# Performance work log

Hardware: AMD Instinct MI355X
Metric: run time of the kernel (lower is better)

## Reference

```python
import jax, jax.numpy as jnp
import numpy as np
from functools import partial

EPS = 1e-5
CHANS = [(3, 64), (64, 64), (64, 128), (128, 128), (128, 256), (256, 256), (256, 256), (256, 256)]

def conv3d(x, w):
    # x: [B,X,Y,Z,Cin], w: [3,3,3,Cin,Cout]; Minkowski stride-1 conv keeps coords -> SAME padding
    return jax.lax.conv_general_dilated(x, w, window_strides=(1, 1, 1), padding='SAME',
                                        dimension_numbers=('NDHWC', 'DHWIO', 'NDHWC'))

def bn(x, g, b):
    # training-mode batch norm over all voxels (MinkowskiBatchNorm forward)
    m = jnp.mean(x, axis=(0, 1, 2, 3))
    v = jnp.var(x, axis=(0, 1, 2, 3))
    return (x - m) * jax.lax.rsqrt(v + EPS) * g + b

def maxpool2(x):
    return jax.lax.reduce_window(x, -jnp.inf, jax.lax.max,
                                 (1, 2, 2, 2, 1), (1, 2, 2, 2, 1), 'VALID')

def setup_inputs() -> dict:
    key = jax.random.key(0)
    ks = jax.random.split(key, 32)
    inp = {'x': jax.random.normal(ks[0], (2, 64, 64, 64, 3), dtype=jnp.float32)}
    for i, (ci, co) in enumerate(CHANS):
        scale = (2.0 / (27 * ci)) ** 0.5  # kaiming for 3x3x3 conv
        inp[f'w{i+1}'] = jax.random.normal(ks[1 + i], (3, 3, 3, ci, co), dtype=jnp.float32) * scale
        inp[f'g{i+1}'] = jnp.ones((co,), dtype=jnp.float32)
        inp[f'b{i+1}'] = jnp.zeros((co,), dtype=jnp.float32)
    inp['wl'] = jax.random.normal(ks[20], (256, 256), dtype=jnp.float32) * (1.0 / 16.0)
    inp['bl'] = jnp.zeros((256,), dtype=jnp.float32)
    return inp

def reference(x, w1, g1, b1, w2, g2, b2, w3, g3, b3, w4, g4, b4,
              w5, g5, b5, w6, g6, b6, w7, g7, b7, w8, g8, b8, wl, bl):
    h = jax.nn.relu(bn(conv3d(x, w1), g1, b1))
    h = jax.nn.relu(bn(conv3d(h, w2), g2, b2))
    h = maxpool2(h)                                   # 64 -> 32
    h = jax.nn.relu(bn(conv3d(h, w3), g3, b3))
    h = jax.nn.relu(bn(conv3d(h, w4), g4, b4))
    h = maxpool2(h)                                   # 32 -> 16
    h = jax.nn.relu(bn(conv3d(h, w5), g5, b5))
    h = jax.nn.relu(bn(conv3d(h, w6), g6, b6))
    h = jax.nn.relu(bn(conv3d(h, w7), g7, b7))
    h = maxpool2(h)                                   # 16 -> 8
    h = bn(conv3d(h, w8), g8, b8)                     # no ReLU before global pool in source
    h = jnp.mean(h, axis=(1, 2, 3))                   # MinkowskiGlobalPooling (avg over coords)
    return h @ wl + bl                                # MinkowskiLinear(256, out_feat)
```

## Files before the change

kernel.cpp:

```cpp
#include <hip/hip_runtime.h>


typedef _Float16 f16;
typedef _Float16 f16x8 __attribute__((ext_vector_type(8)));
typedef _Float16 f16x4 __attribute__((ext_vector_type(4)));
typedef float f32x4 __attribute__((ext_vector_type(4)));

__device__ __forceinline__ int xcd_swz(int bx, int nbx) {
  const int q = nbx >> 3, r = nbx & 7;
  const int x = bx & 7, o = bx >> 3;
  return (x < r ? x * (q + 1) : r * (q + 1) + (x - r) * q) + o;
}

struct WArgs {
  const float* src[8];
  int end[8];
  int S[8], G[8], CR[8], CO[8];
};
__global__ __launch_bounds__(256) void wprep_all(WArgs a, f16* __restrict__ wf)
{
  const int e = blockIdx.x * 256 + threadIdx.x;
  int li = 0;
  while (li < 7 && e >= a.end[li]) ++li;
  if (e >= a.end[li]) return;
  const int base = li ? a.end[li - 1] : 0;
  int x = e - base;
  const int i = x & 7;
  const int l = (x >> 3) & 63;
  int r = x >> 9;
  const int g = r % a.G[li]; r /= a.G[li];
  const int s = r % a.S[li]; r /= a.S[li];
  const int t = r;
  const int k = s * 32 + ((l >> 4) << 3) + i;
  const int co = g * 16 + (l & 15);
  const float v = (k < a.CR[li]) ? a.src[li][((long)t * a.CR[li] + k) * a.CO[li] + co] : 0.f;
  wf[e] = (f16)v;
}

template<int CIN, int CINR, int Z, int WR, int WC, bool HASBN, int SS>
__global__ __launch_bounds__(WR*WC*64) void conv_mfma(
    const void* __restrict__ xin, const f16* __restrict__ wf,
    f16* __restrict__ out, int X, int Y, int Co,
    const float* __restrict__ sc, const float* __restrict__ sh,
    float* __restrict__ part, int partBase,
    float* __restrict__ pout, long outE)
{
  constexpr int NTHR = WR * WC * 64;
  constexpr int L = 64 * WR / Z;
  constexpr int RB = (CIN + 8) * 2;
  constexpr int S = CIN / 32;
  constexpr int COW = 64 * WC;
  constexpr bool SPLIT = (SS > 0);
  __shared__ __align__(16) char slab[(L + 2) * (Z + 2) * RB];
  __shared__ float sstat[WR * WC][2][64];

  const int tid = threadIdx.x;
  const int lane = tid & 63;
  const int wv = tid >> 6;
  const int wr = wv / WC, wc = wv % WC;

  const int bxs = xcd_swz(blockIdx.x, gridDim.x);
  const long vb = (long)bxs * (64 * WR);
  const int XYZ = X * Y * Z;
  const int n = (int)(vb / XYZ);
  const int rem = (int)(vb % XYZ);
  const int x0 = rem / (Y * Z);
  const int y0 = (rem % (Y * Z)) / Z;
  const int co0 = blockIdx.y * COW;
  const int Gtot = Co >> 4;
  const int g0 = (co0 >> 4) + wc * 4;

  int abase[4];
  #pragma unroll
  for (int r = 0; r < 4; ++r) {
    const int vl = wr * 64 + r * 16 + (lane & 15);
    const int ly = vl / Z, z = vl % Z;
    abase[r] = (ly * (Z + 2) + z) * RB + ((lane >> 4) << 4);
  }

  f32x4 acc[4][4];
  const f32x4 fz = {0.f, 0.f, 0.f, 0.f};
  #pragma unroll
  for (int r = 0; r < 4; ++r)
    #pragma unroll
    for (int c = 0; c < 4; ++c) acc[r][c] = fz;

  {
    const f16x8 hz = {};
    for (int e = tid * 8; e < (L + 2) * 2 * CIN; e += NTHR * 8) {
      const int pr = e / CIN, ci = e % CIN;
      const int row = (pr >> 1) * (Z + 2) + (pr & 1) * (Z + 1);
      *(f16x8*)(slab + row * RB + ci * 2) = hz;
    }
  }

  auto stage = [&](int dx) {
    const int xs = x0 + dx - 1;
    const bool xok = (xs >= 0) && (xs < X);
    const long gv0 = ((long)(n * X + xs) * Y + (y0 - 1)) * Z;
    if constexpr (CINR == CIN) {
      const f16* xf = (const f16*)xin;
      constexpr int NE = (L + 2) * Z * CIN;
      for (int e = tid * 8; e < NE; e += NTHR * 8) {
        const int rr = e / CIN, ci = e % CIN;
        const int li = rr / Z, z = rr % Z;
        const int ys = y0 - 1 + li;
        f16x8 h = {};
        if (xok && ys >= 0 && ys < Y) {
          const f16x8 hv = *(const f16x8*)(xf + (gv0 + rr) * CIN + ci);
          if constexpr (HASBN) {
            const float4 s0 = *(const float4*)(sc + ci);
            const float4 s1 = *(const float4*)(sc + ci + 4);
            const float4 h0 = *(const float4*)(sh + ci);
            const float4 h1 = *(const float4*)(sh + ci + 4);
            h[0] = (f16)fmaxf(fmaf((float)hv[0], s0.x, h0.x), 0.f);
            h[1] = (f16)fmaxf(fmaf((float)hv[1], s0.y, h0.y), 0.f);
            h[2] = (f16)fmaxf(fmaf((float)hv[2], s0.z, h0.z), 0.f);
            h[3] = (f16)fmaxf(fmaf((float)hv[3], s0.w, h0.w), 0.f);
            h[4] = (f16)fmaxf(fmaf((float)hv[4], s1.x, h1.x), 0.f);
            h[5] = (f16)fmaxf(fmaf((float)hv[5], s1.y, h1.y), 0.f);
            h[6] = (f16)fmaxf(fmaf((float)hv[6], s1.z, h1.z), 0.f);
            h[7] = (f16)fmaxf(fmaf((float)hv[7], s1.w, h1.w), 0.f);
          } else {
            h = hv;
          }
        }
        *(f16x8*)(slab + (li * (Z + 2) + 1 + z) * RB + ci * 2) = h;
      }
    } else {
      const float* xf = (const float*)xin;
      for (int rr = tid; rr < (L + 2) * Z; rr += NTHR) {
        const int li = rr / Z, z = rr % Z;
        const int ys = y0 - 1 + li;
        f16x8 h = {};
        if (xok && ys >= 0 && ys < Y) {
          const float* p = xf + (gv0 + rr) * CINR;
          #pragma unroll
          for (int i = 0; i < CINR; ++i) h[i] = (f16)p[i];
        }
        char* drow = slab + (li * (Z + 2) + 1 + z) * RB;
        *(f16x8*)drow = h;
        const f16x8 hz = {};
        #pragma unroll
        for (int ch = 1; ch < CIN / 8; ++ch) *(f16x8*)(drow + ch * 16) = hz;
      }
    }
  };

  auto ktaps = [&](int dx, int s) {
    #pragma unroll
    for (int dy = 0; dy < 3; ++dy) {
      #pragma unroll
      for (int dzi = 0; dzi < 3; ++dzi) {
        f16x8 av[4];
        #pragma unroll
        for (int r = 0; r < 4; ++r)
          av[r] = *(const f16x8*)(slab + abase[r] + s * 64 + (dy * (Z + 2) + dzi) * RB);
        const int t = dx * 9 + dy * 3 + dzi;
        f16x8 bv[4];
        #pragma unroll
        for (int c = 0; c < 4; ++c)
          bv[c] = *(const f16x8*)((const char*)wf +
                    (((long)(t * S + s) * Gtot + g0 + c) << 10) + (lane << 4));
        #pragma unroll
        for (int r = 0; r < 4; ++r)
          #pragma unroll
          for (int c = 0; c < 4; ++c)
            acc[r][c] = __builtin_amdgcn_mfma_f32_16x16x32_f16(av[r], bv[c], acc[r][c], 0, 0, 0);
      }
    }
  };

  if constexpr (SPLIT) {
    constexpr int SCH = S / SS;
    const int zb = blockIdx.z;
    const int dx = zb / SS;
    const int s0 = (zb % SS) * SCH;
    stage(dx);
    __syncthreads();
    #pragma unroll
    for (int si = 0; si < SCH; ++si) ktaps(dx, s0 + si);
  } else {
    for (int dx = 0; dx < 3; ++dx) {
      __syncthreads();
      stage(dx);
      __syncthreads();
      for (int s = 0; s < S; ++s) ktaps(dx, s);
    }
  }

  const long vgbase = vb + wr * 64;
  const int cobase = co0 + wc * 64;
  if constexpr (SPLIT) {
    float* pb = pout + (long)blockIdx.z * outE;
    #pragma unroll
    for (int r = 0; r < 4; ++r)
      #pragma unroll
      for (int c = 0; c < 4; ++c)
        #pragma unroll
        for (int q = 0; q < 4; ++q) {
          const long vox = vgbase + r * 16 + ((lane >> 4) << 2) + q;
          const int co = cobase + c * 16 + (lane & 15);
          pb[vox * Co + co] = acc[r][c][q];
        }
    return;
  }

  #pragma unroll
  for (int r = 0; r < 4; ++r)
    #pragma unroll
    for (int c = 0; c < 4; ++c)
      #pragma unroll
      for (int q = 0; q < 4; ++q) {
        const long vox = vgbase + r * 16 + ((lane >> 4) << 2) + q;
        const int co = cobase + c * 16 + (lane & 15);
        out[vox * Co + co] = (f16)acc[r][c][q];
      }

  float s4[4], q4[4];
  #pragma unroll
  for (int c = 0; c < 4; ++c) {
    float s = 0.f, q = 0.f;
    #pragma unroll
    for (int r = 0; r < 4; ++r)
      #pragma unroll
      for (int qd = 0; qd < 4; ++qd) {
        const float v = acc[r][c][qd];
        s += v;
        q = fmaf(v, v, q);
      }
    s4[c] = s; q4[c] = q;
  }
  #pragma unroll
  for (int c = 0; c < 4; ++c) {
    s4[c] += __shfl_xor(s4[c], 16);
    s4[c] += __shfl_xor(s4[c], 32);
    q4[c] += __shfl_xor(q4[c], 16);
    q4[c] += __shfl_xor(q4[c], 32);
  }
  if (lane < 16) {
    #pragma unroll
    for (int c = 0; c < 4; ++c) {
      sstat[wv][0][c * 16 + lane] = s4[c];
      sstat[wv][1][c * 16 + lane] = q4[c];
    }
  }
  __syncthreads();
  const long entry = (long)blockIdx.y * gridDim.x + bxs + partBase;
  for (int t = tid; t < WC * 128; t += NTHR) {
    const int wcc = t >> 7, k = (t >> 6) & 1, ch = t & 63;
    float v = 0.f;
    #pragma unroll
    for (int wr2 = 0; wr2 < WR; ++wr2) v += sstat[wr2 * WC + wcc][k][ch];
    part[entry * (2 * COW) + k * COW + wcc * 64 + ch] = v;
  }
}

__global__ __launch_bounds__(256) void reduce_stats(
    const float* __restrict__ pout, f16* __restrict__ out,
    long outE, int KS, int vpb, float* __restrict__ part)
{
  const int tid = threadIdx.x;
  const int wv = tid >> 6, lane = tid & 63;
  const int vbase = blockIdx.x * vpb;
  float4 s = {0.f, 0.f, 0.f, 0.f}, q = {0.f, 0.f, 0.f, 0.f};
  for (int v = vbase + wv; v < vbase + vpb; v += 4) {
    const long e = (long)v * 256 + lane * 4;
    float4 o = *(const float4*)(pout + e);
    for (int z = 1; z < KS; ++z) {
      const float4 p = *(const float4*)(pout + (long)z * outE + e);
      o.x += p.x; o.y += p.y; o.z += p.z; o.w += p.w;
    }
    f16x4 ov = {(f16)o.x, (f16)o.y, (f16)o.z, (f16)o.w};
    *(f16x4*)(out + e) = ov;
    s.x += o.x; s.y += o.y; s.z += o.z; s.w += o.w;
    q.x = fmaf(o.x, o.x, q.x); q.y = fmaf(o.y, o.y, q.y);
    q.z = fmaf(o.z, o.z, q.z); q.w = fmaf(o.w, o.w, q.w);
  }
  __shared__ float st[4][2][256];
  *(float4*)&st[wv][0][lane * 4] = s;
  *(float4*)&st[wv][1][lane * 4] = q;
  __syncthreads();
  for (int t = tid; t < 512; t += 256) {
    const int k = t >> 8, ch = t & 255;
    part[(long)blockIdx.x * 512 + k * 256 + ch] =
        st[0][k][ch] + st[1][k][ch] + st[2][k][ch] + st[3][k][ch];
  }
}

__global__ __launch_bounds__(256) void stats_final(
    const float* __restrict__ part, int nbx, int CoWin, long nvox,
    const float* __restrict__ g, const float* __restrict__ b,
    float* __restrict__ sc, float* __restrict__ sh)
{
  const int c = blockIdx.x;
  const int by = c / CoWin;
  const int cw = c % CoWin;
  const int tid = threadIdx.x;
  float s = 0.f, ss = 0.f;
  for (int i = tid; i < nbx; i += 256) {
    const long base = ((long)by * nbx + i) * 2 * CoWin;
    s += part[base + cw];
    ss += part[base + CoWin + cw];
  }
  __shared__ float r0[256];
  __shared__ float r1[256];
  r0[tid] = s; r1[tid] = ss;
  __syncthreads();
  #pragma unroll
  for (int o = 128; o > 0; o >>= 1) {
    if (tid < o) { r0[tid] += r0[tid + o]; r1[tid] += r1[tid + o]; }
    __syncthreads();
  }
  if (tid == 0) {
    const float inv = 1.f / (float)nvox;
    const float m = r0[0] * inv;
    const float var = r1[0] * inv - m * m;
    const float scale = rsqrtf(var + 1e-5f) * g[c];
    sc[c] = scale;
    sh[c] = b[c] - m * scale;
  }
}

__global__ __launch_bounds__(256) void maxpool2_aff(
    const f16* __restrict__ in, f16* __restrict__ out,
    int N, int X, int Y, int Z, int C,
    const float* __restrict__ sc, const float* __restrict__ sh)
{
  const int OX = X >> 1, OY = Y >> 1, OZ = Z >> 1;
  const int c4n = C >> 2;
  const long nout = (long)N * OX * OY * OZ * c4n;
  long idx = (long)blockIdx.x * 256 + threadIdx.x;
  if (idx >= nout) return;
  const int c4 = (int)(idx % c4n);
  long v = idx / c4n;
  const int oz = (int)(v % OZ); v /= OZ;
  const int oy = (int)(v % OY); v /= OY;
  const int ox = (int)(v % OX);
  const int n = (int)(v / OX);
  const long sx = (long)Y * Z * C, sy = (long)Z * C, sz = C;
  const long base = ((((long)n * X + 2 * ox) * Y + 2 * oy) * Z + 2 * oz) * (long)C + 4L * c4;
  f16x4 m = *(const f16x4*)(in + base);
  #pragma unroll
  for (int dd = 1; dd < 8; ++dd) {
    const int dxp = dd >> 2, dyp = (dd >> 1) & 1, dzp = dd & 1;
    const f16x4 t = *(const f16x4*)(in + base + dxp * sx + dyp * sy + dzp * sz);
    #pragma unroll
    for (int i = 0; i < 4; ++i) m[i] = (t[i] > m[i]) ? t[i] : m[i];
  }
  const int c = 4 * c4;
  const float4 s4 = *(const float4*)(sc + c);
  const float4 h4 = *(const float4*)(sh + c);
  f16x4 r;
  r[0] = (f16)fmaxf(fmaf((float)m[0], s4.x, h4.x), 0.f);
  r[1] = (f16)fmaxf(fmaf((float)m[1], s4.y, h4.y), 0.f);
  r[2] = (f16)fmaxf(fmaf((float)m[2], s4.z, h4.z), 0.f);
  r[3] = (f16)fmaxf(fmaf((float)m[3], s4.w, h4.w), 0.f);
  *(f16x4*)(out + idx * 4) = r;
}

__global__ __launch_bounds__(256) void head_mean(
    const f16* __restrict__ x8, const float* __restrict__ sc, const float* __restrict__ sh,
    float* __restrict__ hbuf)
{
  const int n = blockIdx.x, cg = blockIdx.y;
  const int tx = threadIdx.x & 63, ty = threadIdx.x >> 6;
  const int c = cg * 64 + tx;
  float s = 0.f;
  for (int v = ty; v < 512; v += 4) s += (float)x8[((long)n * 512 + v) * 256 + c];
  __shared__ float red[4][64];
  red[ty][tx] = s;
  __syncthreads();
  if (ty == 0) {
    s = red[0][tx] + red[1][tx] + red[2][tx] + red[3][tx];
    hbuf[n * 256 + c] = fmaf(s * (1.f / 512.f), sc[c], sh[c]);
  }
}

__global__ __launch_bounds__(256) void head_mv(
    const float* __restrict__ hbuf, const float* __restrict__ wl,
    const float* __restrict__ bl, float* __restrict__ out)
{
  const int n = blockIdx.x, og = blockIdx.y;
  const int tx = threadIdx.x & 63, ty = threadIdx.x >> 6;
  const int oc = og * 64 + tx;
  float a = 0.f;
  const int k0 = ty * 64;
  for (int k = k0; k < k0 + 64; ++k)
    a = fmaf(hbuf[n * 256 + k], wl[(long)k * 256 + oc], a);
  __shared__ float red[4][64];
  red[ty][tx] = a;
  __syncthreads();
  if (ty == 0)
    out[n * 256 + oc] = red[0][tx] + red[1][tx] + red[2][tx] + red[3][tx] + bl[oc];
}

extern "C" void kernel_launch(void* const* d_in, const int* in_sizes, int n_in,
                              void* d_out, int out_size, void* d_ws, size_t ws_size,
                              hipStream_t stream)
{
  const float* x = (const float*)d_in[0];
  const float* W[8];
  const float* G[8];
  const float* B[8];
  for (int i = 0; i < 8; ++i) {
    W[i] = (const float*)d_in[1 + 3 * i];
    G[i] = (const float*)d_in[2 + 3 * i];
    B[i] = (const float*)d_in[3 + 3 * i];
  }
  const float* wl = (const float*)d_in[25];
  const float* bl = (const float*)d_in[26];

  char* ws = (char*)d_ws;
  f16*   A    = (f16*)ws;
  f16*   Bb   = (f16*)(ws + (64L << 20));
  float* pK   = (float*)(ws + (128L << 20));
  float* part = (float*)(ws + (152L << 20));
  float* scb  = part + 262144L;
  float* shb  = scb + 2048L;
  float* hbuf = shb + 2048L;
  f16*   wfb  = (f16*)(hbuf + 512L);

  const int wfS[8]  = {1, 2, 2, 4, 4, 8, 8, 8};
  const int wfG[8]  = {4, 4, 8, 8, 16, 16, 16, 16};
  const int wfCR[8] = {3, 64, 64, 128, 128, 256, 256, 256};
  const int wfCO[8] = {64, 64, 128, 128, 256, 256, 256, 256};
  long wfOff[9];
  wfOff[0] = 0;
  for (int i = 0; i < 8; ++i) wfOff[i + 1] = wfOff[i] + 27L * wfS[i] * wfG[i] * 512;
  if (ws_size < (size_t)((char*)(wfb + wfOff[8]) - ws)) return;
  auto WF = [&](int i) { return wfb + wfOff[i]; };
  auto SC = [&](int i) { return scb + i * 256; };
  auto SH = [&](int i) { return shb + i * 256; };

  {
    WArgs a;
    for (int i = 0; i < 8; ++i) {
      a.src[i] = W[i]; a.end[i] = (int)wfOff[i + 1];
      a.S[i] = wfS[i]; a.G[i] = wfG[i]; a.CR[i] = wfCR[i]; a.CO[i] = wfCO[i];
    }
    wprep_all<<<(unsigned)((wfOff[8] + 255) / 256), 256, 0, stream>>>(a, wfb);
  }

  auto fin = [&](int layer, int nbx, int CoWin, int C, long nvox) {
    stats_final<<<C, 256, 0, stream>>>(part, nbx, CoWin, nvox,
                                       G[layer], B[layer], SC(layer), SH(layer));
  };
  auto pool_aff = [&](const f16* in, f16* ob, int N, int Xd, int Yd, int Zd, int C, int layer) {
    const long nout = (long)N * (Xd / 2) * (Yd / 2) * (Zd / 2) * (C / 4);
    maxpool2_aff<<<(unsigned)((nout + 255) / 256), 256, 0, stream>>>(
        in, ob, N, Xd, Yd, Zd, C, SC(layer), SH(layer));
  };

  conv_mfma<32, 3, 64, 4, 1, false, 0><<<dim3(2048, 1), 256, 0, stream>>>(
      x, WF(0), A, 64, 64, 64, nullptr, nullptr, part, 0, nullptr, 0);
  fin(0, 2048, 64, 64, 524288);
  conv_mfma<64, 64, 64, 4, 1, true, 0><<<dim3(2048, 1), 256, 0, stream>>>(
      A, WF(1), Bb, 64, 64, 64, SC(0), SH(0), part, 0, nullptr, 0);
  fin(1, 2048, 64, 64, 524288);
  pool_aff(Bb, A, 2, 64, 64, 64, 64, 1);

  conv_mfma<64, 64, 32, 2, 2, false, 0><<<dim3(512, 1), 256, 0, stream>>>(
      A, WF(2), Bb, 32, 32, 128, nullptr, nullptr, part, 0, nullptr, 0);
  fin(2, 512, 128, 128, 65536);
  conv_mfma<128, 128, 32, 2, 2, true, 0><<<dim3(512, 1), 256, 0, stream>>>(
      Bb, WF(3), A, 32, 32, 128, SC(2), SH(2), part, 0, nullptr, 0);
  fin(3, 512, 128, 128, 65536);
  pool_aff(A, Bb, 2, 32, 32, 32, 128, 3);

  const long E16 = 2097152;
  conv_mfma<128, 128, 16, 1, 4, false, 1><<<dim3(128, 1, 3), 256, 0, stream>>>(
      Bb, WF(4), nullptr, 16, 16, 256, nullptr, nullptr, nullptr, 0, pK, E16);
  reduce_stats<<<256, 256, 0, stream>>>(pK, A, E16, 3, 32, part);
  fin(4, 256, 256, 256, 8192);
  conv_mfma<256, 256, 16, 1, 4, true, 1><<<dim3(128, 1, 3), 256, 0, stream>>>(
      A, WF(5), nullptr, 16, 16, 256, SC(4), SH(4), nullptr, 0, pK, E16);
  reduce_stats<<<256, 256, 0, stream>>>(pK, Bb, E16, 3, 32, part);
  fin(5, 256, 256, 256, 8192);
  conv_mfma<256, 256, 16, 1, 4, true, 1><<<dim3(128, 1, 3), 256, 0, stream>>>(
      Bb, WF(6), nullptr, 16, 16, 256, SC(5), SH(5), nullptr, 0, pK, E16);
  reduce_stats<<<256, 256, 0, stream>>>(pK, A, E16, 3, 32, part);
  fin(6, 256, 256, 256, 8192);
  pool_aff(A, Bb, 2, 16, 16, 16, 256, 6);

  const long E8 = 262144;
  conv_mfma<256, 256, 8, 1, 4, false, 4><<<dim3(16, 1, 12), 256, 0, stream>>>(
      Bb, WF(7), nullptr, 8, 8, 256, nullptr, nullptr, nullptr, 0, pK, E8);
  reduce_stats<<<256, 256, 0, stream>>>(pK, A, E8, 12, 4, part);
  fin(7, 256, 256, 256, 1024);

  head_mean<<<dim3(2, 4), 256, 0, stream>>>(A, SC(7), SH(7), hbuf);
  head_mv<<<dim3(2, 4), 256, 0, stream>>>(hbuf, wl, bl, (float*)d_out);
}
```

Measured before the change: 563.0 us.

## Pack first-layer conv taps into K dimension and prefetch slab staging through registers

```diff
diff --git a/kernel.cpp b/kernel.cpp
--- a/kernel.cpp
+++ b/kernel.cpp
@@ -33,13 +33,157 @@
   const int t = r;
   const int k = s * 32 + ((l >> 4) << 3) + i;
   const int co = g * 16 + (l & 15);
-  const float v = (k < a.CR[li]) ? a.src[li][((long)t * a.CR[li] + k) * a.CO[li] + co] : 0.f;
+  float v;
+  if (li == 0) {
+    const int tap = k >> 3, ci = k & 7;
+    v = (ci < 3 && tap < 27) ? a.src[0][((long)tap * 3 + ci) * 64 + co] : 0.f;
+  } else {
+    v = (k < a.CR[li]) ? a.src[li][((long)t * a.CR[li] + k) * a.CO[li] + co] : 0.f;
+  }
   wf[e] = (f16)v;
 }
 
-template<int CIN, int CINR, int Z, int WR, int WC, bool HASBN, int SS>
+__global__ __launch_bounds__(256) void conv1_mfma(
+    const float* __restrict__ xin, const f16* __restrict__ wf,
+    f16* __restrict__ out, float* __restrict__ part)
+{
+  constexpr int Z = 64, Y = 64, X = 64, L = 4;
+  constexpr int RB = 48;
+  constexpr int SLAB = (L + 2) * (Z + 2) * RB;
+  __shared__ __align__(16) char slab[3 * SLAB];
+  __shared__ float sstat[4][2][64];
+
+  const int tid = threadIdx.x;
+  const int lane = tid & 63;
+  const int wr = tid >> 6;
+
+  const int bxs = xcd_swz(blockIdx.x, gridDim.x);
+  const long vb = (long)bxs * 256;
+  const int n = (int)(vb >> 18);
+  const int rem = (int)(vb & 262143);
+  const int x0 = rem >> 12;
+  const int y0 = (rem >> 6) & 63;
+
+  if (tid < 36) {
+    const int s = tid / 12, pr = tid % 12;
+    const int row = (pr >> 1) * (Z + 2) + (pr & 1) * (Z + 1);
+    const f16x8 hz = {};
+    *(f16x8*)(slab + s * SLAB + row * RB) = hz;
+  }
+
+  for (int rr2 = tid; rr2 < 3 * (L + 2) * Z; rr2 += 256) {
+    const int s = rr2 / ((L + 2) * Z);
+    const int rr = rr2 % ((L + 2) * Z);
+    const int li = rr / Z, z = rr % Z;
+    const int xs = x0 + s - 1, ys = y0 - 1 + li;
+    f16x8 h = {};
+    if (xs >= 0 && xs < X && ys >= 0 && ys < Y) {
+      const float* p = xin + (((long)(n * X + xs) * Y + ys) * Z + z) * 3;
+      h[0] = (f16)p[0]; h[1] = (f16)p[1]; h[2] = (f16)p[2];
+    }
+    *(f16x8*)(slab + s * SLAB + (li * (Z + 2) + 1 + z) * RB) = h;
+  }
+
+  int abase[4];
+  #pragma unroll
+  for (int r = 0; r < 4; ++r) {
+    const int vl = wr * 64 + r * 16 + (lane & 15);
+    abase[r] = ((vl >> 6) * (Z + 2) + (vl & 63)) * RB;
+  }
+  const int c = lane >> 4;
+  int rofftab[7];
+  #pragma unroll
+  for (int j = 0; j < 7; ++j) {
+    const int tap = 4 * j + c;
+    if (tap < 27) {
+      const int dx = tap / 9, dy = (tap / 3) % 3, dz = tap % 3;
+      rofftab[j] = dx * SLAB + (dy * (Z + 2) + dz) * RB;
+    } else {
+      rofftab[j] = 0;
+    }
+  }
+
+  f32x4 acc[4][4];
+  const f32x4 fz = {0.f, 0.f, 0.f, 0.f};
+  #pragma unroll
+  for (int r = 0; r < 4; ++r)
+    #pragma unroll
+    for (int cc = 0; cc < 4; ++cc) acc[r][cc] = fz;
+
+  __syncthreads();
+
+  #pragma unroll
+  for (int j = 0; j < 7; ++j) {
+    f16x8 av[4];
+    #pragma unroll
+    for (int r = 0; r < 4; ++r)
+      av[r] = *(const f16x8*)(slab + abase[r] + rofftab[j]);
+    f16x8 bv[4];
+    #pragma unroll
+    for (int c2 = 0; c2 < 4; ++c2)
+      bv[c2] = *(const f16x8*)((const char*)wf + ((j * 4 + c2) << 10) + (lane << 4));
+    __builtin_amdgcn_s_setprio(1);
+    #pragma unroll
+    for (int r = 0; r < 4; ++r)
+      #pragma unroll
+      for (int c2 = 0; c2 < 4; ++c2)
+        acc[r][c2] = __builtin_amdgcn_mfma_f32_16x16x32_f16(av[r], bv[c2], acc[r][c2], 0, 0, 0);
+    __builtin_amdgcn_s_setprio(0);
+  }
+
+  const long vgbase = vb + wr * 64;
+  #pragma unroll
+  for (int r = 0; r < 4; ++r)
+    #pragma unroll
+    for (int cc = 0; cc < 4; ++cc)
+      #pragma unroll
+      for (int q = 0; q < 4; ++q) {
+        const long vox = vgbase + r * 16 + ((lane >> 4) << 2) + q;
+        const int co = cc * 16 + (lane & 15);
+        out[vox * 64 + co] = (f16)acc[r][cc][q];
+      }
+
+  float s4[4], q4[4];
+  #pragma unroll
+  for (int cc = 0; cc < 4; ++cc) {
+    float s = 0.f, q = 0.f;
+    #pragma unroll
+    for (int r = 0; r < 4; ++r)
+      #pragma unroll
+      for (int qd = 0; qd < 4; ++qd) {
+        const float v = acc[r][cc][qd];
+        s += v;
+        q = fmaf(v, v, q);
+      }
+    s4[cc] = s; q4[cc] = q;
+  }
+  #pragma unroll
+  for (int cc = 0; cc < 4; ++cc) {
+    s4[cc] += __shfl_xor(s4[cc], 16);
+    s4[cc] += __shfl_xor(s4[cc], 32);
+    q4[cc] += __shfl_xor(q4[cc], 16);
+    q4[cc] += __shfl_xor(q4[cc], 32);
+  }
+  if (lane < 16) {
+    #pragma unroll
+    for (int cc = 0; cc < 4; ++cc) {
+      sstat[wr][0][cc * 16 + lane] = s4[cc];
+      sstat[wr][1][cc * 16 + lane] = q4[cc];
+    }
+  }
+  __syncthreads();
+  for (int t = tid; t < 128; t += 256) {
+    const int k = (t >> 6) & 1, ch = t & 63;
+    float v = 0.f;
+    #pragma unroll
+    for (int w2 = 0; w2 < 4; ++w2) v += sstat[w2][k][ch];
+    part[(long)bxs * 128 + k * 64 + ch] = v;
+  }
+}
+
+template<int CIN, int Z, int WR, int WC, bool HASBN, int SS>
 __global__ __launch_bounds__(WR*WC*64) void conv_mfma(
-    const void* __restrict__ xin, const f16* __restrict__ wf,
+    const f16* __restrict__ xin, const f16* __restrict__ wf,
     f16* __restrict__ out, int X, int Y, int Co,
     const float* __restrict__ sc, const float* __restrict__ sh,
     float* __restrict__ part, int partBase,
@@ -51,6 +195,9 @@
   constexpr int S = CIN / 32;
   constexpr int COW = 64 * WC;
   constexpr bool SPLIT = (SS > 0);
+  constexpr int NE = (L + 2) * Z * CIN;
+  constexpr int NLD = NE / (NTHR * 8);
+  static_assert(NE % (NTHR * 8) == 0, "staging not divisible");
   __shared__ __align__(16) char slab[(L + 2) * (Z + 2) * RB];
   __shared__ float sstat[WR * WC][2][64];
 
@@ -94,56 +241,51 @@
     }
   }
 
-  auto stage = [&](int dx) {
+  f16x8 regs[NLD];
+
+  auto LOAD = [&](int dx) {
     const int xs = x0 + dx - 1;
     const bool xok = (xs >= 0) && (xs < X);
     const long gv0 = ((long)(n * X + xs) * Y + (y0 - 1)) * Z;
-    if constexpr (CINR == CIN) {
-      const f16* xf = (const f16*)xin;
-      constexpr int NE = (L + 2) * Z * CIN;
-      for (int e = tid * 8; e < NE; e += NTHR * 8) {
-        const int rr = e / CIN, ci = e % CIN;
-        const int li = rr / Z, z = rr % Z;
-        const int ys = y0 - 1 + li;
-        f16x8 h = {};
+    #pragma unroll
+    for (int j = 0; j < NLD; ++j) {
+      const int e = tid * 8 + j * NTHR * 8;
+      const int rr = e / CIN;
+      const int ys = y0 - 1 + rr / Z;
+      f16x8 h = {};
+      if (xok && ys >= 0 && ys < Y)
+        h = *(const f16x8*)(xin + (gv0 + rr) * CIN + (e % CIN));
+      regs[j] = h;
+    }
+  };
+
+  auto WRITE = [&](int dx) {
+    const int xs = x0 + dx - 1;
+    const bool xok = (xs >= 0) && (xs < X);
+    #pragma unroll
+    for (int j = 0; j < NLD; ++j) {
+      const int e = tid * 8 + j * NTHR * 8;
+      const int rr = e / CIN, ci = e % CIN;
+      const int li = rr / Z, z = rr % Z;
+      const int ys = y0 - 1 + li;
+      f16x8 h = regs[j];
+      if constexpr (HASBN) {
         if (xok && ys >= 0 && ys < Y) {
-          const f16x8 hv = *(const f16x8*)(xf + (gv0 + rr) * CIN + ci);
-          if constexpr (HASBN) {
-            const float4 s0 = *(const float4*)(sc + ci);
-            const float4 s1 = *(const float4*)(sc + ci + 4);
-            const float4 h0 = *(const float4*)(sh + ci);
-            const float4 h1 = *(const float4*)(sh + ci + 4);
-            h[0] = (f16)fmaxf(fmaf((float)hv[0], s0.x, h0.x), 0.f);
-            h[1] = (f16)fmaxf(fmaf((float)hv[1], s0.y, h0.y), 0.f);
-            h[2] = (f16)fmaxf(fmaf((float)hv[2], s0.z, h0.z), 0.f);
-            h[3] = (f16)fmaxf(fmaf((float)hv[3], s0.w, h0.w), 0.f);
-            h[4] = (f16)fmaxf(fmaf((float)hv[4], s1.x, h1.x), 0.f);
-            h[5] = (f16)fmaxf(fmaf((float)hv[5], s1.y, h1.y), 0.f);
-            h[6] = (f16)fmaxf(fmaf((float)hv[6], s1.z, h1.z), 0.f);
-            h[7] = (f16)fmaxf(fmaf((float)hv[7], s1.w, h1.w), 0.f);
-          } else {
-            h = hv;
-          }
+          const float4 s0 = *(const float4*)(sc + ci);
+          const float4 s1 = *(const float4*)(sc + ci + 4);
+          const float4 h0 = *(const float4*)(sh + ci);
+          const float4 h1 = *(const float4*)(sh + ci + 4);
+          h[0] = (f16)fmaxf(fmaf((float)h[0], s0.x, h0.x), 0.f);
+          h[1] = (f16)fmaxf(fmaf((float)h[1], s0.y, h0.y), 0.f);
+          h[2] = (f16)fmaxf(fmaf((float)h[2], s0.z, h0.z), 0.f);
+          h[3] = (f16)fmaxf(fmaf((float)h[3], s0.w, h0.w), 0.f);
+          h[4] = (f16)fmaxf(fmaf((float)h[4], s1.x, h1.x), 0.f);
+          h[5] = (f16)fmaxf(fmaf((float)h[5], s1.y, h1.y), 0.f);
+          h[6] = (f16)fmaxf(fmaf((float)h[6], s1.z, h1.z), 0.f);
+          h[7] = (f16)fmaxf(fmaf((float)h[7], s1.w, h1.w), 0.f);
         }
-        *(f16x8*)(slab + (li * (Z + 2) + 1 + z) * RB + ci * 2) = h;
       }
-    } else {
-      const float* xf = (const float*)xin;
-      for (int rr = tid; rr < (L + 2) * Z; rr += NTHR) {
-        const int li = rr / Z, z = rr % Z;
-        const int ys = y0 - 1 + li;
-        f16x8 h = {};
-        if (xok && ys >= 0 && ys < Y) {
-          const float* p = xf + (gv0 + rr) * CINR;
-          #pragma unroll
-          for (int i = 0; i < CINR; ++i) h[i] = (f16)p[i];
-        }
-        char* drow = slab + (li * (Z + 2) + 1 + z) * RB;
-        *(f16x8*)drow = h;
-        const f16x8 hz = {};
-        #pragma unroll
-        for (int ch = 1; ch < CIN / 8; ++ch) *(f16x8*)(drow + ch * 16) = hz;
-      }
+      *(f16x8*)(slab + (li * (Z + 2) + 1 + z) * RB + ci * 2) = h;
     }
   };
 
@@ -162,11 +304,13 @@
         for (int c = 0; c < 4; ++c)
           bv[c] = *(const f16x8*)((const char*)wf +
                     (((long)(t * S + s) * Gtot + g0 + c) << 10) + (lane << 4));
+        __builtin_amdgcn_s_setprio(1);
         #pragma unroll
         for (int r = 0; r < 4; ++r)
           #pragma unroll
           for (int c = 0; c < 4; ++c)
             acc[r][c] = __builtin_amdgcn_mfma_f32_16x16x32_f16(av[r], bv[c], acc[r][c], 0, 0, 0);
+        __builtin_amdgcn_s_setprio(0);
       }
     }
   };
@@ -176,16 +320,20 @@
     const int zb = blockIdx.z;
     const int dx = zb / SS;
     const int s0 = (zb % SS) * SCH;
-    stage(dx);
+    LOAD(dx);
+    WRITE(dx);
     __syncthreads();
     #pragma unroll
     for (int si = 0; si < SCH; ++si) ktaps(dx, s0 + si);
   } else {
+    LOAD(0);
+    WRITE(0);
+    __syncthreads();
     for (int dx = 0; dx < 3; ++dx) {
+      if (dx < 2) LOAD(dx + 1);
+      for (int s = 0; s < S; ++s) ktaps(dx, s);
       __syncthreads();
-      stage(dx);
-      __syncthreads();
-      for (int s = 0; s < S; ++s) ktaps(dx, s);
+      if (dx < 2) { WRITE(dx + 1); __syncthreads(); }
     }
   }
 
@@ -421,13 +569,14 @@
   float* hbuf = shb + 2048L;
   f16*   wfb  = (f16*)(hbuf + 512L);
 
-  const int wfS[8]  = {1, 2, 2, 4, 4, 8, 8, 8};
+  const int wfS[8]  = {7, 2, 2, 4, 4, 8, 8, 8};
   const int wfG[8]  = {4, 4, 8, 8, 16, 16, 16, 16};
+  const int wfT[8]  = {1, 27, 27, 27, 27, 27, 27, 27};
   const int wfCR[8] = {3, 64, 64, 128, 128, 256, 256, 256};
   const int wfCO[8] = {64, 64, 128, 128, 256, 256, 256, 256};
   long wfOff[9];
   wfOff[0] = 0;
-  for (int i = 0; i < 8; ++i) wfOff[i + 1] = wfOff[i] + 27L * wfS[i] * wfG[i] * 512;
+  for (int i = 0; i < 8; ++i) wfOff[i + 1] = wfOff[i] + (long)wfT[i] * wfS[i] * wfG[i] * 512;
   if (ws_size < (size_t)((char*)(wfb + wfOff[8]) - ws)) return;
   auto WF = [&](int i) { return wfb + wfOff[i]; };
   auto SC = [&](int i) { return scb + i * 256; };
@@ -452,39 +601,38 @@
         in, ob, N, Xd, Yd, Zd, C, SC(layer), SH(layer));
   };
 
-  conv_mfma<32, 3, 64, 4, 1, false, 0><<<dim3(2048, 1), 256, 0, stream>>>(
-      x, WF(0), A, 64, 64, 64, nullptr, nullptr, part, 0, nullptr, 0);
+  conv1_mfma<<<2048, 256, 0, stream>>>(x, WF(0), A, part);
   fin(0, 2048, 64, 64, 524288);
-  conv_mfma<64, 64, 64, 4, 1, true, 0><<<dim3(2048, 1), 256, 0, stream>>>(
+  conv_mfma<64, 64, 4, 1, true, 0><<<dim3(2048, 1), 256, 0, stream>>>(
       A, WF(1), Bb, 64, 64, 64, SC(0), SH(0), part, 0, nullptr, 0);
   fin(1, 2048, 64, 64, 524288);
   pool_aff(Bb, A, 2, 64, 64, 64, 64, 1);
 
-  conv_mfma<64, 64, 32, 2, 2, false, 0><<<dim3(512, 1), 256, 0, stream>>>(
+  conv_mfma<64, 32, 2, 2, false, 0><<<dim3(512, 1), 256, 0, stream>>>(
       A, WF(2), Bb, 32, 32, 128, nullptr, nullptr, part, 0, nullptr, 0);
   fin(2, 512, 128, 128, 65536);
-  conv_mfma<128, 128, 32, 2, 2, true, 0><<<dim3(512, 1), 256, 0, stream>>>(
+  conv_mfma<128, 32, 2, 2, true, 0><<<dim3(512, 1), 256, 0, stream>>>(
       Bb, WF(3), A, 32, 32, 128, SC(2), SH(2), part, 0, nullptr, 0);
   fin(3, 512, 128, 128, 65536);
   pool_aff(A, Bb, 2, 32, 32, 32, 128, 3);
 
   const long E16 = 2097152;
-  conv_mfma<128, 128, 16, 1, 4, false, 1><<<dim3(128, 1, 3), 256, 0, stream>>>(
+  conv_mfma<128, 16, 1, 4, false, 1><<<dim3(128, 1, 3), 256, 0, stream>>>(
       Bb, WF(4), nullptr, 16, 16, 256, nullptr, nullptr, nullptr, 0, pK, E16);
   reduce_stats<<<256, 256, 0, stream>>>(pK, A, E16, 3, 32, part);
   fin(4, 256, 256, 256, 8192);
-  conv_mfma<256, 256, 16, 1, 4, true, 1><<<dim3(128, 1, 3), 256, 0, stream>>>(
+  conv_mfma<256, 16, 1, 4, true, 1><<<dim3(128, 1, 3), 256, 0, stream>>>(
       A, WF(5), nullptr, 16, 16, 256, SC(4), SH(4), nullptr, 0, pK, E16);
   reduce_stats<<<256, 256, 0, stream>>>(pK, Bb, E16, 3, 32, part);
   fin(5, 256, 256, 256, 8192);
-  conv_mfma<256, 256, 16, 1, 4, true, 1><<<dim3(128, 1, 3), 256, 0, stream>>>(
+  conv_mfma<256, 16, 1, 4, true, 1><<<dim3(128, 1, 3), 256, 0, stream>>>(
       Bb, WF(6), nullptr, 16, 16, 256, SC(5), SH(5), nullptr, 0, pK, E16);
   reduce_stats<<<256, 256, 0, stream>>>(pK, A, E16, 3, 32, part);
   fin(6, 256, 256, 256, 8192);
   pool_aff(A, Bb, 2, 16, 16, 16, 256, 6);
 
   const long E8 = 262144;
-  conv_mfma<256, 256, 8, 1, 4, false, 4><<<dim3(16, 1, 12), 256, 0, stream>>>(
+  conv_mfma<256, 8, 1, 4, false, 4><<<dim3(16, 1, 12), 256, 0, stream>>>(
       Bb, WF(7), nullptr, 8, 8, 256, nullptr, nullptr, nullptr, 0, pK, E8);
   reduce_stats<<<256, 256, 0, stream>>>(pK, A, E8, 12, 4, part);
   fin(7, 256, 256, 256, 1024);
```

After: 591.5 us. +5.1%, slower.
